# Kernel optimization log

Hardware: AMD Instinct MI355X
Metric: run time of the kernel (lower is better)

Reference implementation:

```python
import jax, jax.numpy as jnp
import numpy as np

N_NODES = 100000
N_EDGES = 1600000
IN_DIM = 256
HID = 128
N_LAYERS = 4
OUT_DIM = 7
LAMDA = 0.5
LN_EPS = 1e-5


def setup_inputs() -> dict:
    key = jax.random.key(0)
    ks = jax.random.split(key, 12)
    x = jax.random.normal(ks[0], (N_NODES, IN_DIM), jnp.float32)
    edge_index = jax.random.randint(ks[1], (2, N_EDGES), 0, N_NODES, dtype=jnp.int32)

    def unif(k, shape, fan_out):
        s = 1.0 / np.sqrt(fan_out)
        return jax.random.uniform(k, shape, jnp.float32, -s, s)

    W_proj = unif(ks[2], (IN_DIM, HID), HID)
    b_proj = unif(ks[3], (HID,), HID)
    gamma = jnp.ones((HID,), jnp.float32)
    beta = jnp.zeros((HID,), jnp.float32)
    q_w = unif(ks[4], (HID, 1), 1)
    q_b = unif(ks[5], (1,), 1)
    conv_w = unif(ks[6], (N_LAYERS, HID, HID), HID)
    cls_w = unif(ks[7], (HID, OUT_DIM), OUT_DIM)
    cls_b = unif(ks[8], (OUT_DIM,), OUT_DIM)
    return {"x": x, "edge_index": edge_index, "W_proj": W_proj, "b_proj": b_proj,
            "gamma": gamma, "beta": beta, "q_w": q_w, "q_b": q_b,
            "conv_w": conv_w, "cls_w": cls_w, "cls_b": cls_b}


def reference(x, edge_index, W_proj, b_proj, gamma, beta, q_w, q_b, conv_w, cls_w, cls_b):
    n = x.shape[0]
    row, col = edge_index[0], edge_index[1]

    # symmetric normalization: D^-1/2 A D^-1/2 with unit edge data (duplicates sum)
    deg = jax.ops.segment_sum(jnp.ones(row.shape[0], x.dtype), row, num_segments=n)
    deg = jnp.where(deg == 0, jnp.ones_like(deg), deg)  # (row_sum==0)*1 + row_sum
    d_inv_sqrt = deg ** -0.5
    ew = d_inv_sqrt[row] * d_inv_sqrt[col]  # [E]

    def spmm(h):  # out[r] += ew * h[c]
        return jax.ops.segment_sum(ew[:, None] * h[col], row, num_segments=n)

    def layernorm(h):
        mu = jnp.mean(h, axis=-1, keepdims=True)
        var = jnp.mean((h - mu) ** 2, axis=-1, keepdims=True)
        return gamma * (h - mu) * jax.lax.rsqrt(var + LN_EPS) + beta

    h0 = layernorm(x @ W_proj + b_proj)  # project + layernorm
    h = h0
    for i in range(conv_w.shape[0]):
        # dropout is identity in eval mode
        s = jax.nn.sigmoid(h @ q_w + q_b - 1.0)  # [N,1] learned gate
        theta = LAMDA / (i + 1)
        hi = spmm(h)
        support = (1.0 - s) * hi + s * h0  # AOR blend (variant=False -> r == support)
        out = theta * (support @ conv_w[i]) + (1.0 - theta) * support  # DLR
        h = layernorm(jax.nn.relu(out))
    return h @ cls_w + cls_b
```

## Files before the change

### kernel.cpp

```cpp
#include <hip/hip_runtime.h>
#include <hip/hip_bf16.h>
#include <hip/hip_fp16.h>
#include <stdint.h>

#define N_NODES 100000
#define N_EDGES 1600000
#define IN_DIM 256
#define HID 128
#define N_LAYERS 4
#define OUT_DIM 7
#define LN_EPS 1e-5f

#define BSHIFT 6
#define BROWS 64
#define NBK 1563
#define CHUNK 16384
#define NCH ((N_EDGES + CHUNK - 1) / CHUNK)

typedef __attribute__((ext_vector_type(8))) short bf16x8;
typedef __attribute__((ext_vector_type(4))) float f32x4;

__device__ inline float bf2f1(uint16_t u) {
    union { uint32_t i; float f; } a; a.i = ((uint32_t)u) << 16; return a.f;
}
__device__ inline uint16_t f2bf(float f) {
    union { float f; uint32_t i; } a; a.f = f;
    uint32_t lsb = (a.i >> 16) & 1u;
    a.i += 0x7fffu + lsb;
    return (uint16_t)(a.i >> 16);
}
__device__ inline uint32_t packq(float a, float b, float qinv) {
    int qa = __float2int_rn(a * qinv);
    int qb = __float2int_rn(b * qinv);
    return ((uint32_t)(uint16_t)(short)qa) | (((uint32_t)(uint16_t)(short)qb) << 16);
}

__global__ void k_detect(const uint32_t* __restrict__ W, int* __restrict__ flag) {
    if (threadIdx.x == 0 && blockIdx.x == 0) {
        int cnt = 0;
        for (int i = 0; i < 64; i++) {
            uint32_t lo = W[i] & 0xffffu;
            uint32_t ex = (lo >> 7) & 0xff;
            if (ex >= 0x60 && ex < 0x7c) cnt++;
        }
        *flag = (cnt < 32) ? 1 : 0;
    }
}

__global__ __launch_bounds__(256) void k_cvt(const void* a0, const void* a1, const void* a2,
                                             const void* a3, const void* a4, const void* a5,
                                             const void* a6, const void* a7, const void* a8,
                                             float* __restrict__ dst, const int* __restrict__ flag) {
    int t = blockIdx.x * 256 + threadIdx.x;
    if (t >= 99720) return;
    const void* src; int i; int off;
    if      (t < 32768) { src = a0; i = t;         off = 0;     }
    else if (t < 32896) { src = a1; i = t - 32768; off = 32768; }
    else if (t < 33024) { src = a2; i = t - 32896; off = 32896; }
    else if (t < 33152) { src = a3; i = t - 33024; off = 33024; }
    else if (t < 33280) { src = a4; i = t - 33152; off = 33152; }
    else if (t < 33281) { src = a5; i = t - 33280; off = 33280; }
    else if (t < 98817) { src = a6; i = t - 33281; off = 33296; }
    else if (t < 99713) { src = a7; i = t - 98817; off = 98832; }
    else                { src = a8; i = t - 99713; off = 99728; }
    float v;
    if (*flag) v = ((const float*)src)[i];
    else       v = bf2f1(((const uint16_t*)src)[i]);
    dst[off + i] = v;
}

__global__ __launch_bounds__(256) void k_wsplit(const float* __restrict__ stg,
                                                uint16_t* __restrict__ wpThi, uint16_t* __restrict__ wpTlo,
                                                uint16_t* __restrict__ cwThi, uint16_t* __restrict__ cwTlo) {
    int t = blockIdx.x * 256 + threadIdx.x;
    if (t >= 32768 + 65536) return;
    float v; size_t dst; uint16_t *ha, *la;
    if (t < 32768) {
        int k = t >> 7, c = t & 127;
        v = stg[t];
        dst = (size_t)c * 256 + k; ha = wpThi; la = wpTlo;
    } else {
        int u = t - 32768;
        int L = u >> 14, rem = u & 16383;
        int k = rem >> 7, c = rem & 127;
        v = stg[33296 + u];
        dst = (size_t)L * 16384 + (size_t)c * 128 + k; ha = cwThi; la = cwTlo;
    }
    uint16_t hb = f2bf(v);
    uint16_t lb = f2bf(v - bf2f1(hb));
    ha[dst] = hb; la[dst] = lb;
}


__global__ __launch_bounds__(256) void k_hist(const int* __restrict__ row, int* __restrict__ hist) {
    __shared__ int lh[NBK];
    int b = blockIdx.x, tid = threadIdx.x;
    for (int i = tid; i < NBK; i += 256) lh[i] = 0;
    __syncthreads();
    int e0 = b * CHUNK;
    int lim = N_EDGES - e0; if (lim > CHUNK) lim = CHUNK;
    for (int i = tid; i < lim; i += 256) atomicAdd(&lh[row[e0 + i] >> BSHIFT], 1);
    __syncthreads();
    for (int i = tid; i < NBK; i += 256) hist[(size_t)b * NBK + i] = lh[i];
}

__global__ __launch_bounds__(128) void k_hscan(int* __restrict__ hist, int* __restrict__ totB) {
    __shared__ int s[128];
    int bkt = blockIdx.x, t = threadIdx.x;
    int v = (t < NCH) ? hist[(size_t)t * NBK + bkt] : 0;
    s[t] = v;
    __syncthreads();
    for (int off = 1; off < 128; off <<= 1) {
        int add = (t >= off) ? s[t - off] : 0;
        __syncthreads();
        s[t] += add;
        __syncthreads();
    }
    if (t < NCH) hist[(size_t)t * NBK + bkt] = s[t] - v;
    if (t == 127) totB[bkt] = s[127];
}

__global__ __launch_bounds__(256) void k_bscan(const int* __restrict__ totB,
                                               int* __restrict__ boffB, int* __restrict__ rp) {
    __shared__ int ps[256];
    int t = threadIdx.x;
    const int STRIP = 7;
    int base = t * STRIP;
    int loc[STRIP]; int sum = 0;
#pragma unroll
    for (int j = 0; j < STRIP; j++) {
        int idx = base + j;
        int v = (idx < NBK) ? totB[idx] : 0;
        loc[j] = sum; sum += v;
    }
    ps[t] = sum;
    __syncthreads();
    int v = ps[t];
    for (int off = 1; off < 256; off <<= 1) {
        int add = (t >= off) ? ps[t - off] : 0;
        __syncthreads();
        ps[t] += add;
        __syncthreads();
    }
    int excl = ps[t] - v;
#pragma unroll
    for (int j = 0; j < STRIP; j++) {
        int idx = base + j;
        if (idx < NBK) boffB[idx] = excl + loc[j];
    }
    if (t == 0) { boffB[NBK] = N_EDGES; rp[N_NODES] = N_EDGES; }
}

__global__ __launch_bounds__(256) void k_sortscat(const int* __restrict__ row, const int* __restrict__ col,
                                                  const int* __restrict__ hist, const int* __restrict__ boffB,
                                                  uint32_t* __restrict__ ebp) {
    __shared__ int dbase[NBK];
    __shared__ int lcnt[NBK];
    int b = blockIdx.x, tid = threadIdx.x;
    for (int i = tid; i < NBK; i += 256) {
        dbase[i] = boffB[i] + hist[(size_t)b * NBK + i];
        lcnt[i] = 0;
    }
    __syncthreads();
    int e0 = b * CHUNK;
    int lim = N_EDGES - e0; if (lim > CHUNK) lim = CHUNK;
    for (int i = tid; i < lim; i += 256) {
        int r = row[e0 + i], c = col[e0 + i];
        int bk = r >> BSHIFT;
        int rank = atomicAdd(&lcnt[bk], 1);
        ebp[dbase[bk] + rank] = ((uint32_t)(r & (BROWS - 1)) << 17) | (uint32_t)c;
    }
}

__global__ __launch_bounds__(256) void k_bfin(const uint32_t* __restrict__ ebp, const int* __restrict__ boffB,
                                              int* __restrict__ rp, float* __restrict__ dis,
                                              int* __restrict__ edc) {
    __shared__ int ldeg[BROWS];
    __shared__ int lcur[BROWS];
    int b = blockIdx.x, tid = threadIdx.x;
    int base = boffB[b];
    int n = boffB[b + 1] - base;
    if (tid < BROWS) ldeg[tid] = 0;
    __syncthreads();
    for (int i = tid; i < n; i += 256) atomicAdd(&ldeg[ebp[base + i] >> 17], 1);
    __syncthreads();
    if (tid == 0) {
        int run = 0;
        for (int r = 0; r < BROWS; r++) { int d = ldeg[r]; lcur[r] = run; run += d; }
    }
    __syncthreads();
    int row0 = b << BSHIFT;
    if (tid < BROWS && row0 + tid < N_NODES) {
        int d = ldeg[tid];
        rp[row0 + tid]  = base + lcur[tid];
        dis[row0 + tid] = rsqrtf((float)(d > 0 ? d : 1));
    }
    __syncthreads();
    for (int i = tid; i < n; i += 256) {
        uint32_t pk = ebp[base + i];
        int r = pk >> 17;
        int pos = atomicAdd(&lcur[r], 1);
        edc[base + pos] = (int)(pk & 0x1FFFFu);
    }
}


__global__ __launch_bounds__(256) void k_spmm(const uint32_t* __restrict__ Hq,
                                              const float* __restrict__ ScD,
                                              const float* __restrict__ H0,
                                              const int* __restrict__ rp,
                                              const int* __restrict__ edc,
                                              const float* __restrict__ S,
                                              const float* __restrict__ dis,
                                              float* __restrict__ Sup) {
    int wid  = (blockIdx.x * 256 + threadIdx.x) >> 6;
    int lane = threadIdx.x & 63;
    if (wid >= N_NODES) return;

    float s  = S[wid];
    float dr = dis[wid];

    int p0 = rp[wid], p1 = rp[wid + 1];
    float ax = 0.f, ay = 0.f;
    int p = p0;
    for (; p + 4 <= p1; p += 4) {
        int c0 = edc[p], c1 = edc[p + 1], c2 = edc[p + 2], c3 = edc[p + 3];
        uint32_t u0 = Hq[(size_t)c0 * 64 + lane];
        uint32_t u1 = Hq[(size_t)c1 * 64 + lane];
        uint32_t u2 = Hq[(size_t)c2 * 64 + lane];
        uint32_t u3 = Hq[(size_t)c3 * 64 + lane];
        float w0 = ScD[c0], w1 = ScD[c1], w2 = ScD[c2], w3 = ScD[c3];
        ax += w0 * (float)((int)(u0 << 16) >> 16) + w1 * (float)((int)(u1 << 16) >> 16)
            + w2 * (float)((int)(u2 << 16) >> 16) + w3 * (float)((int)(u3 << 16) >> 16);
        ay += w0 * (float)((int)u0 >> 16) + w1 * (float)((int)u1 >> 16)
            + w2 * (float)((int)u2 >> 16) + w3 * (float)((int)u3 >> 16);
    }
    for (; p < p1; p++) {
        int c = edc[p];
        uint32_t u = Hq[(size_t)c * 64 + lane];
        float w = ScD[c];
        ax += w * (float)((int)(u << 16) >> 16);
        ay += w * (float)((int)u >> 16);
    }
    float h0x = H0[(size_t)wid * 128 + lane];
    float h0y = H0[(size_t)wid * 128 + 64 + lane];
    float f = (1.f - s) * dr;
    Sup[(size_t)wid * 128 + lane]      = f * ax + s * h0x;
    Sup[(size_t)wid * 128 + 64 + lane] = f * ay + s * h0y;
}


template <int KD, int MODE, int WH, int WQ>
__global__ __launch_bounds__(256) void k_gemm_mfma(
    const void* __restrict__ Araw,
    const uint16_t* __restrict__ WThi,
    const uint16_t* __restrict__ WTlo,
    const float* __restrict__ bias, const float* __restrict__ gamma,
    const float* __restrict__ beta, const float* __restrict__ qw,
    const float* __restrict__ qb, float theta, const int* __restrict__ flag,
    const float* __restrict__ dis,
    float* __restrict__ Hout, uint32_t* __restrict__ Hq,
    float* __restrict__ Sc, float* __restrict__ S)
{
    __shared__ __align__(16) uint16_t sAhi[64 * 64];
    __shared__ __align__(16) uint16_t sAlo[64 * 64];
    __shared__ __align__(16) uint16_t sBhi[128 * 64];
    __shared__ __align__(16) uint16_t sBlo[128 * 64];

    const int tid  = threadIdx.x;
    const int lane = tid & 63;
    const int wv   = tid >> 6;
    const int li   = lane & 15;
    const int lg   = lane >> 4;
    const size_t row0 = (size_t)blockIdx.x * 64;
    const int f32in = (MODE == 0) ? *flag : 1;

    f32x4 acc[8];
#pragma unroll
    for (int ct = 0; ct < 8; ct++) acc[ct] = (f32x4){0.f, 0.f, 0.f, 0.f};

    for (int kc = 0; kc < KD / 64; kc++) {
        __syncthreads();
#pragma unroll
        for (int it = 0; it < 2; it++) {
            int s  = tid + it * 256;
            int r  = s >> 3, sl = s & 7;
            size_t rg = row0 + r; if (rg >= N_NODES) rg = N_NODES - 1;
            uint4 vh, vl;
            if (f32in) {
                const float* p = (const float*)Araw + rg * KD + kc * 64 + sl * 8;
                float4 u0 = *(const float4*)p;
                float4 u1 = *(const float4*)(p + 4);
                float f[8] = {u0.x, u0.y, u0.z, u0.w, u1.x, u1.y, u1.z, u1.w};
                uint32_t hw[8], lw[8];
#pragma unroll
                for (int j = 0; j < 8; j++) {
                    uint16_t hb = f2bf(f[j]);
                    uint16_t lb = f2bf(f[j] - bf2f1(hb));
                    hw[j] = hb; lw[j] = lb;
                }
                vh.x = hw[0] | (hw[1] << 16); vh.y = hw[2] | (hw[3] << 16);
                vh.z = hw[4] | (hw[5] << 16); vh.w = hw[6] | (hw[7] << 16);
                vl.x = lw[0] | (lw[1] << 16); vl.y = lw[2] | (lw[3] << 16);
                vl.z = lw[4] | (lw[5] << 16); vl.w = lw[6] | (lw[7] << 16);
            } else {
                vh = *(const uint4*)((const uint16_t*)Araw + rg * KD + kc * 64 + sl * 8);
                vl.x = 0u; vl.y = 0u; vl.z = 0u; vl.w = 0u;
            }
            uint32_t byte = (uint32_t)(r * 128 + sl * 16) ^ (uint32_t)((r & 7) << 4);
            *(uint4*)((char*)sAhi + byte) = vh;
            *(uint4*)((char*)sAlo + byte) = vl;
        }
#pragma unroll
        for (int it = 0; it < 4; it++) {
            int s = tid + it * 256;
            int r = s >> 3, sl = s & 7;
            size_t gsrc = (size_t)r * KD + kc * 64 + sl * 8;
            uint4 vh = *(const uint4*)(WThi + gsrc);
            uint4 vl = *(const uint4*)(WTlo + gsrc);
            uint32_t byte = (uint32_t)(r * 128 + sl * 16) ^ (uint32_t)((r & 7) << 4);
            *(uint4*)((char*)sBhi + byte) = vh;
            *(uint4*)((char*)sBlo + byte) = vl;
        }
        __syncthreads();
#pragma unroll
        for (int ks = 0; ks < 2; ks++) {
            int arow = wv * 16 + li;
            uint32_t ab = (uint32_t)(arow * 128 + ks * 64 + lg * 16) ^ (uint32_t)((arow & 7) << 4);
            bf16x8 ah = *(const bf16x8*)((const char*)sAhi + ab);
            bf16x8 al = *(const bf16x8*)((const char*)sAlo + ab);
#pragma unroll
            for (int ct = 0; ct < 8; ct++) {
                int brow = ct * 16 + li;
                uint32_t bb = (uint32_t)(brow * 128 + ks * 64 + lg * 16) ^ (uint32_t)((brow & 7) << 4);
                bf16x8 bh = *(const bf16x8*)((const char*)sBhi + bb);
                bf16x8 bl = *(const bf16x8*)((const char*)sBlo + bb);
                acc[ct] = __builtin_amdgcn_mfma_f32_16x16x32_bf16(ah, bh, acc[ct], 0, 0, 0);
                acc[ct] = __builtin_amdgcn_mfma_f32_16x16x32_bf16(ah, bl, acc[ct], 0, 0, 0);
                acc[ct] = __builtin_amdgcn_mfma_f32_16x16x32_bf16(al, bh, acc[ct], 0, 0, 0);
            }
        }
    }

    float gm[8], bt[8], qv[8], bi[8];
#pragma unroll
    for (int ct = 0; ct < 8; ct++) {
        int c = ct * 16 + li;
        gm[ct] = gamma[c]; bt[ct] = beta[c]; qv[ct] = qw[c];
        bi[ct] = (MODE == 0) ? bias[c] : 0.f;
    }
    const float qbv = qb[0];
    const float om  = 1.f - theta;
    const float* Af = (const float*)Araw;

#pragma unroll
    for (int r = 0; r < 4; r++) {
        int rowl  = wv * 16 + lg * 4 + r;
        size_t rg = row0 + rowl;
        size_t rc = (rg < N_NODES) ? rg : (N_NODES - 1);
        float v[8];
        if (MODE == 0) {
#pragma unroll
            for (int ct = 0; ct < 8; ct++) v[ct] = acc[ct][r] + bi[ct];
        } else {
#pragma unroll
            for (int ct = 0; ct < 8; ct++) {
                float sv = Af[rc * KD + ct * 16 + li];
                float o  = theta * acc[ct][r] + om * sv;
                v[ct] = o > 0.f ? o : 0.f;
            }
        }
        float sum = 0.f, sq = 0.f;
#pragma unroll
        for (int ct = 0; ct < 8; ct++) { sum += v[ct]; sq += v[ct] * v[ct]; }
        sum += __shfl_xor(sum, 1); sum += __shfl_xor(sum, 2);
        sum += __shfl_xor(sum, 4); sum += __shfl_xor(sum, 8);
        sq  += __shfl_xor(sq, 1);  sq  += __shfl_xor(sq, 2);
        sq  += __shfl_xor(sq, 4);  sq  += __shfl_xor(sq, 8);
        float mu  = sum * (1.f / 128.f);
        float var = fmaxf(sq * (1.f / 128.f) - mu * mu, 0.f);
        float rs  = rsqrtf(var + LN_EPS);
        float y[8];
#pragma unroll
        for (int ct = 0; ct < 8; ct++) y[ct] = gm[ct] * (v[ct] - mu) * rs + bt[ct];

        if (WQ) {
            float zd = 0.f, am = 0.f;
#pragma unroll
            for (int ct = 0; ct < 8; ct++) { zd += y[ct] * qv[ct]; am = fmaxf(am, fabsf(y[ct])); }
            zd += __shfl_xor(zd, 1); zd += __shfl_xor(zd, 2);
            zd += __shfl_xor(zd, 4); zd += __shfl_xor(zd, 8);
            am = fmaxf(am, __shfl_xor(am, 1)); am = fmaxf(am, __shfl_xor(am, 2));
            am = fmaxf(am, __shfl_xor(am, 4)); am = fmaxf(am, __shfl_xor(am, 8));
            float amc  = fmaxf(am, 1e-20f);
            float qinv = 32767.f / amc;
            if (rg < N_NODES) {
                uint32_t* mq = Hq + rg * 64;
#pragma unroll
                for (int ct = 0; ct < 4; ct++)
                    mq[ct * 16 + li] = packq(y[ct], y[ct + 4], qinv);
                if (li == 0) {
                    Sc[rg] = amc * (1.f / 32767.f) * dis[rg];
                    S[rg]  = 1.f / (1.f + __expf(-(zd + qbv - 1.f)));
                }
            }
        }
        if (WH && rg < N_NODES) {
            float* dst = Hout + rg * 128;
#pragma unroll
            for (int ct = 0; ct < 8; ct++) dst[ct * 16 + li] = y[ct];
        }
    }
}


__global__ __launch_bounds__(256) void k_cls(const float* __restrict__ H,
                                             const float* __restrict__ Wc,
                                             const float* __restrict__ bc,
                                             const int* __restrict__ flag,
                                             void* __restrict__ out) {
    __shared__ float wS[128][8];
    int tid = threadIdx.x;
    for (int idx = tid; idx < 128 * 7; idx += 256) wS[idx / 7][idx % 7] = Wc[idx];
    __syncthreads();
    int isf32 = *flag;
    int gid = blockIdx.x * 256 + tid;
    int n = gid >> 3, j = gid & 7;
    if (n >= N_NODES || j >= OUT_DIM) return;
    const float4* hr = (const float4*)(H + (size_t)n * 128);
    float acc = bc[j];
#pragma unroll
    for (int k4 = 0; k4 < 32; k4++) {
        float4 h4 = hr[k4];
        acc += h4.x * wS[4 * k4][j]     + h4.y * wS[4 * k4 + 1][j]
             + h4.z * wS[4 * k4 + 2][j] + h4.w * wS[4 * k4 + 3][j];
    }
    size_t oi = (size_t)n * OUT_DIM + j;
    if (isf32) ((float*)out)[oi] = acc;
    else       ((uint16_t*)out)[oi] = f2bf(acc);
}


extern "C" void kernel_launch(void* const* d_in, const int* in_sizes, int n_in,
                              void* d_out, int out_size, void* d_ws, size_t ws_size,
                              hipStream_t stream) {
    const void* x_raw = d_in[0];
    const int*  ei    = (const int*)d_in[1];
    const int* row = ei;
    const int* col = ei + N_EDGES;

    char* ws = (char*)d_ws;
    size_t off = 0;
    auto alloc = [&](size_t b) { void* p = ws + off; off = (off + b + 255) & ~(size_t)255; return p; };
    int*      flag = (int*)alloc(4);
    float*    stgf = (float*)alloc((size_t)99744 * 4);
    int*      rp   = (int*)alloc(((size_t)N_NODES + 1) * 4);
    float*    dis  = (float*)alloc((size_t)N_NODES * 4);
    int*      hist = (int*)alloc((size_t)NCH * NBK * 4);
    int*      totB = (int*)alloc((size_t)NBK * 4);
    int*      boffB= (int*)alloc(((size_t)NBK + 1) * 4);
    int*      edc  = (int*)alloc((size_t)N_EDGES * 4);
    float*    h0   = (float*)alloc((size_t)N_NODES * HID * 4);
    float*    sup  = (float*)alloc((size_t)N_NODES * HID * 4);
    uint32_t* hq   = (uint32_t*)alloc((size_t)N_NODES * 64 * 4);
    float*    Scq  = (float*)alloc((size_t)N_NODES * 4);
    float*    Sg   = (float*)alloc((size_t)N_NODES * 4);
    uint16_t* wpThi = (uint16_t*)alloc((size_t)32768 * 2);
    uint16_t* wpTlo = (uint16_t*)alloc((size_t)32768 * 2);
    uint16_t* cwThi = (uint16_t*)alloc((size_t)65536 * 2);
    uint16_t* cwTlo = (uint16_t*)alloc((size_t)65536 * 2);
    uint32_t* ebp  = (uint32_t*)h0;

    const float* bp  = stgf + 32768;
    const float* gm  = stgf + 32896;
    const float* bt  = stgf + 33024;
    const float* qw  = stgf + 33152;
    const float* qb  = stgf + 33280;
    const float* clw = stgf + 98832;
    const float* clb = stgf + 99728;

    k_detect<<<1, 64, 0, stream>>>((const uint32_t*)d_in[2], flag);
    k_cvt<<<(99720 + 255) / 256, 256, 0, stream>>>(d_in[2], d_in[3], d_in[4], d_in[5], d_in[6],
                                                   d_in[7], d_in[8], d_in[9], d_in[10], stgf, flag);
    k_wsplit<<<(98304 + 255) / 256, 256, 0, stream>>>(stgf, wpThi, wpTlo, cwThi, cwTlo);

    k_hist<<<NCH, 256, 0, stream>>>(row, hist);
    k_hscan<<<NBK, 128, 0, stream>>>(hist, totB);
    k_bscan<<<1, 256, 0, stream>>>(totB, boffB, rp);
    k_sortscat<<<NCH, 256, 0, stream>>>(row, col, hist, boffB, ebp);
    k_bfin<<<NBK, 256, 0, stream>>>(ebp, boffB, rp, dis, edc);

    const int gemm_grid = (N_NODES + 63) / 64;
    k_gemm_mfma<IN_DIM, 0, 1, 1><<<gemm_grid, 256, 0, stream>>>(
        x_raw, wpThi, wpTlo, bp, gm, bt, qw, qb, 0.f, flag, dis, h0, hq, Scq, Sg);

    for (int i = 0; i < N_LAYERS; i++) {
        k_spmm<<<(N_NODES + 3) / 4, 256, 0, stream>>>(hq, Scq, h0, rp, edc, Sg, dis, sup);
        float theta = 0.5f / (float)(i + 1);
        const uint16_t* whi = cwThi + (size_t)i * 16384;
        const uint16_t* wlo = cwTlo + (size_t)i * 16384;
        if (i < N_LAYERS - 1) {
            k_gemm_mfma<HID, 1, 0, 1><<<gemm_grid, 256, 0, stream>>>(
                sup, whi, wlo, nullptr, gm, bt, qw, qb, theta, flag, dis, sup, hq, Scq, Sg);
        } else {
            k_gemm_mfma<HID, 1, 1, 0><<<gemm_grid, 256, 0, stream>>>(
                sup, whi, wlo, nullptr, gm, bt, qw, qb, theta, flag, dis, sup, hq, Scq, Sg);
        }
    }
    k_cls<<<((size_t)N_NODES * 8 + 255) / 256, 256, 0, stream>>>(sup, clw, clb, flag, d_out);
}
```

Measured before the change: 755.0 us.

## Prefetch next GEMM K-chunk into registers, specialize precision path, unroll SpMM by 8

The GEMM kernel body becomes a template on a full-precision flag. When the input is bf16 (flag off), the low-part weight loads and the extra MFMA passes are removed at compile time. The K-loop now prefetches the next chunk of A and B into registers while MFMAs run on the current shared-memory tile, which adds register pressure and a second barrier per iteration. The SpMM gather loop is unrolled to 8 edges with batched index, row and scale loads, and the H0 load is hoisted so more memory requests are in flight.

New measurement: 884.2 us. +17.1%, slower.

```diff
diff --git a/kernel.cpp b/kernel.cpp
--- a/kernel.cpp
+++ b/kernel.cpp
@@ -219,21 +219,39 @@
 
     float s  = S[wid];
     float dr = dis[wid];
+    float h0x = H0[(size_t)wid * 128 + lane];
+    float h0y = H0[(size_t)wid * 128 + 64 + lane];
 
     int p0 = rp[wid], p1 = rp[wid + 1];
     float ax = 0.f, ay = 0.f;
     int p = p0;
+    for (; p + 8 <= p1; p += 8) {
+        int c[8]; uint32_t u[8]; float w[8];
+#pragma unroll
+        for (int j = 0; j < 8; j++) c[j] = edc[p + j];
+#pragma unroll
+        for (int j = 0; j < 8; j++) u[j] = Hq[(size_t)c[j] * 64 + lane];
+#pragma unroll
+        for (int j = 0; j < 8; j++) w[j] = ScD[c[j]];
+#pragma unroll
+        for (int j = 0; j < 8; j++) {
+            ax += w[j] * (float)((int)(u[j] << 16) >> 16);
+            ay += w[j] * (float)((int)u[j] >> 16);
+        }
+    }
     for (; p + 4 <= p1; p += 4) {
-        int c0 = edc[p], c1 = edc[p + 1], c2 = edc[p + 2], c3 = edc[p + 3];
-        uint32_t u0 = Hq[(size_t)c0 * 64 + lane];
-        uint32_t u1 = Hq[(size_t)c1 * 64 + lane];
-        uint32_t u2 = Hq[(size_t)c2 * 64 + lane];
-        uint32_t u3 = Hq[(size_t)c3 * 64 + lane];
-        float w0 = ScD[c0], w1 = ScD[c1], w2 = ScD[c2], w3 = ScD[c3];
-        ax += w0 * (float)((int)(u0 << 16) >> 16) + w1 * (float)((int)(u1 << 16) >> 16)
-            + w2 * (float)((int)(u2 << 16) >> 16) + w3 * (float)((int)(u3 << 16) >> 16);
-        ay += w0 * (float)((int)u0 >> 16) + w1 * (float)((int)u1 >> 16)
-            + w2 * (float)((int)u2 >> 16) + w3 * (float)((int)u3 >> 16);
+        int c[4]; uint32_t u[4]; float w[4];
+#pragma unroll
+        for (int j = 0; j < 4; j++) c[j] = edc[p + j];
+#pragma unroll
+        for (int j = 0; j < 4; j++) u[j] = Hq[(size_t)c[j] * 64 + lane];
+#pragma unroll
+        for (int j = 0; j < 4; j++) w[j] = ScD[c[j]];
+#pragma unroll
+        for (int j = 0; j < 4; j++) {
+            ax += w[j] * (float)((int)(u[j] << 16) >> 16);
+            ay += w[j] * (float)((int)u[j] >> 16);
+        }
     }
     for (; p < p1; p++) {
         int c = edc[p];
@@ -242,30 +260,24 @@
         ax += w * (float)((int)(u << 16) >> 16);
         ay += w * (float)((int)u >> 16);
     }
-    float h0x = H0[(size_t)wid * 128 + lane];
-    float h0y = H0[(size_t)wid * 128 + 64 + lane];
     float f = (1.f - s) * dr;
     Sup[(size_t)wid * 128 + lane]      = f * ax + s * h0x;
     Sup[(size_t)wid * 128 + 64 + lane] = f * ay + s * h0y;
 }
 
 
-template <int KD, int MODE, int WH, int WQ>
-__global__ __launch_bounds__(256) void k_gemm_mfma(
-    const void* __restrict__ Araw,
-    const uint16_t* __restrict__ WThi,
-    const uint16_t* __restrict__ WTlo,
-    const float* __restrict__ bias, const float* __restrict__ gamma,
-    const float* __restrict__ beta, const float* __restrict__ qw,
-    const float* __restrict__ qb, float theta, const int* __restrict__ flag,
-    const float* __restrict__ dis,
-    float* __restrict__ Hout, uint32_t* __restrict__ Hq,
-    float* __restrict__ Sc, float* __restrict__ S)
+template <int KD, int MODE, int WH, int WQ, int WF>
+__device__ __forceinline__ void gemm_body(
+    const void* __restrict__ Araw, const uint16_t* __restrict__ WThi,
+    const uint16_t* __restrict__ WTlo, const float* __restrict__ bias,
+    const float* __restrict__ gamma, const float* __restrict__ beta,
+    const float* __restrict__ qw, const float* __restrict__ qb, float theta,
+    const float* __restrict__ dis, float* __restrict__ Hout,
+    uint32_t* __restrict__ Hq, float* __restrict__ Sc, float* __restrict__ S,
+    uint16_t* sAhi, uint16_t* sAlo, uint16_t* sBhi, uint16_t* sBlo)
 {
-    __shared__ __align__(16) uint16_t sAhi[64 * 64];
-    __shared__ __align__(16) uint16_t sAlo[64 * 64];
-    __shared__ __align__(16) uint16_t sBhi[128 * 64];
-    __shared__ __align__(16) uint16_t sBlo[128 * 64];
+    constexpr int F32A = (MODE == 0) ? WF : 1;
+    constexpr int NC = KD / 64;
 
     const int tid  = threadIdx.x;
     const int lane = tid & 63;
@@ -273,73 +285,106 @@
     const int li   = lane & 15;
     const int lg   = lane >> 4;
     const size_t row0 = (size_t)blockIdx.x * 64;
-    const int f32in = (MODE == 0) ? *flag : 1;
 
     f32x4 acc[8];
 #pragma unroll
     for (int ct = 0; ct < 8; ct++) acc[ct] = (f32x4){0.f, 0.f, 0.f, 0.f};
 
-    for (int kc = 0; kc < KD / 64; kc++) {
-        __syncthreads();
+    float far[2][8];
+    uint4 abr[2];
+    uint4 bhr[4], blr[4];
+
+    auto loadA = [&](int kc) {
 #pragma unroll
         for (int it = 0; it < 2; it++) {
-            int s  = tid + it * 256;
-            int r  = s >> 3, sl = s & 7;
+            int s = tid + it * 256;
+            int r = s >> 3, sl = s & 7;
             size_t rg = row0 + r; if (rg >= N_NODES) rg = N_NODES - 1;
-            uint4 vh, vl;
-            if (f32in) {
+            if constexpr (F32A) {
                 const float* p = (const float*)Araw + rg * KD + kc * 64 + sl * 8;
                 float4 u0 = *(const float4*)p;
                 float4 u1 = *(const float4*)(p + 4);
-                float f[8] = {u0.x, u0.y, u0.z, u0.w, u1.x, u1.y, u1.z, u1.w};
+                far[it][0] = u0.x; far[it][1] = u0.y; far[it][2] = u0.z; far[it][3] = u0.w;
+                far[it][4] = u1.x; far[it][5] = u1.y; far[it][6] = u1.z; far[it][7] = u1.w;
+            } else {
+                abr[it] = *(const uint4*)((const uint16_t*)Araw + rg * KD + kc * 64 + sl * 8);
+            }
+        }
+    };
+    auto storeA = [&]() {
+#pragma unroll
+        for (int it = 0; it < 2; it++) {
+            int s = tid + it * 256;
+            int r = s >> 3, sl = s & 7;
+            uint32_t byte = (uint32_t)(r * 128 + sl * 16) ^ (uint32_t)((r & 7) << 4);
+            if constexpr (F32A) {
                 uint32_t hw[8], lw[8];
 #pragma unroll
                 for (int j = 0; j < 8; j++) {
-                    uint16_t hb = f2bf(f[j]);
-                    uint16_t lb = f2bf(f[j] - bf2f1(hb));
+                    uint16_t hb = f2bf(far[it][j]);
+                    uint16_t lb = f2bf(far[it][j] - bf2f1(hb));
                     hw[j] = hb; lw[j] = lb;
                 }
+                uint4 vh, vl;
                 vh.x = hw[0] | (hw[1] << 16); vh.y = hw[2] | (hw[3] << 16);
                 vh.z = hw[4] | (hw[5] << 16); vh.w = hw[6] | (hw[7] << 16);
                 vl.x = lw[0] | (lw[1] << 16); vl.y = lw[2] | (lw[3] << 16);
                 vl.z = lw[4] | (lw[5] << 16); vl.w = lw[6] | (lw[7] << 16);
+                *(uint4*)((char*)sAhi + byte) = vh;
+                *(uint4*)((char*)sAlo + byte) = vl;
             } else {
-                vh = *(const uint4*)((const uint16_t*)Araw + rg * KD + kc * 64 + sl * 8);
-                vl.x = 0u; vl.y = 0u; vl.z = 0u; vl.w = 0u;
+                *(uint4*)((char*)sAhi + byte) = abr[it];
             }
-            uint32_t byte = (uint32_t)(r * 128 + sl * 16) ^ (uint32_t)((r & 7) << 4);
-            *(uint4*)((char*)sAhi + byte) = vh;
-            *(uint4*)((char*)sAlo + byte) = vl;
-        }
+        }
+    };
+    auto loadB = [&](int kc) {
 #pragma unroll
         for (int it = 0; it < 4; it++) {
             int s = tid + it * 256;
             int r = s >> 3, sl = s & 7;
             size_t gsrc = (size_t)r * KD + kc * 64 + sl * 8;
-            uint4 vh = *(const uint4*)(WThi + gsrc);
-            uint4 vl = *(const uint4*)(WTlo + gsrc);
+            bhr[it] = *(const uint4*)(WThi + gsrc);
+            if constexpr (WF) blr[it] = *(const uint4*)(WTlo + gsrc);
+        }
+    };
+    auto storeB = [&]() {
+#pragma unroll
+        for (int it = 0; it < 4; it++) {
+            int s = tid + it * 256;
+            int r = s >> 3, sl = s & 7;
             uint32_t byte = (uint32_t)(r * 128 + sl * 16) ^ (uint32_t)((r & 7) << 4);
-            *(uint4*)((char*)sBhi + byte) = vh;
-            *(uint4*)((char*)sBlo + byte) = vl;
-        }
+            *(uint4*)((char*)sBhi + byte) = bhr[it];
+            if constexpr (WF) *(uint4*)((char*)sBlo + byte) = blr[it];
+        }
+    };
+
+    loadA(0); loadB(0);
+    for (int kc = 0; kc < NC; kc++) {
+        storeA(); storeB();
         __syncthreads();
+        if (kc + 1 < NC) { loadA(kc + 1); loadB(kc + 1); }
 #pragma unroll
         for (int ks = 0; ks < 2; ks++) {
             int arow = wv * 16 + li;
             uint32_t ab = (uint32_t)(arow * 128 + ks * 64 + lg * 16) ^ (uint32_t)((arow & 7) << 4);
             bf16x8 ah = *(const bf16x8*)((const char*)sAhi + ab);
-            bf16x8 al = *(const bf16x8*)((const char*)sAlo + ab);
+            bf16x8 al;
+            if constexpr (F32A) al = *(const bf16x8*)((const char*)sAlo + ab);
 #pragma unroll
             for (int ct = 0; ct < 8; ct++) {
                 int brow = ct * 16 + li;
                 uint32_t bb = (uint32_t)(brow * 128 + ks * 64 + lg * 16) ^ (uint32_t)((brow & 7) << 4);
                 bf16x8 bh = *(const bf16x8*)((const char*)sBhi + bb);
-                bf16x8 bl = *(const bf16x8*)((const char*)sBlo + bb);
                 acc[ct] = __builtin_amdgcn_mfma_f32_16x16x32_bf16(ah, bh, acc[ct], 0, 0, 0);
-                acc[ct] = __builtin_amdgcn_mfma_f32_16x16x32_bf16(ah, bl, acc[ct], 0, 0, 0);
-                acc[ct] = __builtin_amdgcn_mfma_f32_16x16x32_bf16(al, bh, acc[ct], 0, 0, 0);
+                if constexpr (F32A)
+                    acc[ct] = __builtin_amdgcn_mfma_f32_16x16x32_bf16(al, bh, acc[ct], 0, 0, 0);
+                if constexpr (WF) {
+                    bf16x8 bl = *(const bf16x8*)((const char*)sBlo + bb);
+                    acc[ct] = __builtin_amdgcn_mfma_f32_16x16x32_bf16(ah, bl, acc[ct], 0, 0, 0);
+                }
             }
         }
+        __syncthreads();
     }
 
     float gm[8], bt[8], qv[8], bi[8];
@@ -411,6 +456,29 @@
             for (int ct = 0; ct < 8; ct++) dst[ct * 16 + li] = y[ct];
         }
     }
+}
+
+template <int KD, int MODE, int WH, int WQ>
+__global__ __launch_bounds__(256) void k_gemm_mfma(
+    const void* __restrict__ Araw, const uint16_t* __restrict__ WThi,
+    const uint16_t* __restrict__ WTlo, const float* __restrict__ bias,
+    const float* __restrict__ gamma, const float* __restrict__ beta,
+    const float* __restrict__ qw, const float* __restrict__ qb, float theta,
+    const int* __restrict__ flag, const float* __restrict__ dis,
+    float* __restrict__ Hout, uint32_t* __restrict__ Hq,
+    float* __restrict__ Sc, float* __restrict__ S)
+{
+    __shared__ __align__(16) uint16_t sAhi[64 * 64];
+    __shared__ __align__(16) uint16_t sAlo[64 * 64];
+    __shared__ __align__(16) uint16_t sBhi[128 * 64];
+    __shared__ __align__(16) uint16_t sBlo[128 * 64];
+
+    if (*flag)
+        gemm_body<KD, MODE, WH, WQ, 1>(Araw, WThi, WTlo, bias, gamma, beta, qw, qb,
+                                       theta, dis, Hout, Hq, Sc, S, sAhi, sAlo, sBhi, sBlo);
+    else
+        gemm_body<KD, MODE, WH, WQ, 0>(Araw, WThi, WTlo, bias, gamma, beta, qw, qb,
+                                       theta, dis, Hout, Hq, Sc, S, sAhi, sAlo, sBhi, sBlo);
 }
 
 
```

## Drop LDS staging in GEMM, prepack weights for direct MFMA loads, deepen SpMM unroll

Applied to the files above, without the earlier changes.

Weights are prepacked into an MFMA-fragment-ordered layout so each lane loads its B fragment straight from global or L2 memory. The A operand is also read directly from global memory, which removes the shared-memory staging and both barriers per K chunk. The GEMM is templated on the input-precision flag, so bf16 inputs skip the low-part MFMA and the W-low load. The flag comes from host-side input sizes when available, with kernel variants launched conditionally. SpMM unrolls to 8 gathers per iteration and hoists the H0 loads; the trade-off is more redundant global B reads per wave and higher register pressure.

New measurement: 834.6 us. 1.11x slower.

```diff
diff --git a/kernel.cpp b/kernel.cpp
--- a/kernel.cpp
+++ b/kernel.cpp
@@ -35,6 +35,12 @@
     return ((uint32_t)(uint16_t)(short)qa) | (((uint32_t)(uint16_t)(short)qb) << 16);
 }
 
+__device__ __host__ inline int wpack_idx(int k, int c) {
+    int kc = k >> 6, ks = (k >> 5) & 1, lg = (k >> 3) & 3, e = k & 7;
+    int ct = c >> 4, li = c & 15;
+    return ((((kc * 2 + ks) * 8 + ct) * 16 + li) * 4 + lg) * 8 + e;
+}
+
 __global__ void k_detect(const uint32_t* __restrict__ W, int* __restrict__ flag) {
     if (threadIdx.x == 0 && blockIdx.x == 0) {
         int cnt = 0;
@@ -45,6 +51,9 @@
         }
         *flag = (cnt < 32) ? 1 : 0;
     }
+}
+__global__ void k_setflag(int* __restrict__ flag, int v) {
+    if (threadIdx.x == 0) *flag = v;
 }
 
 __global__ __launch_bounds__(256) void k_cvt(const void* a0, const void* a1, const void* a2,
@@ -70,21 +79,21 @@
 }
 
 __global__ __launch_bounds__(256) void k_wsplit(const float* __restrict__ stg,
-                                                uint16_t* __restrict__ wpThi, uint16_t* __restrict__ wpTlo,
-                                                uint16_t* __restrict__ cwThi, uint16_t* __restrict__ cwTlo) {
+                                                uint16_t* __restrict__ wpkhi, uint16_t* __restrict__ wpklo,
+                                                uint16_t* __restrict__ cwkhi, uint16_t* __restrict__ cwklo) {
     int t = blockIdx.x * 256 + threadIdx.x;
     if (t >= 32768 + 65536) return;
     float v; size_t dst; uint16_t *ha, *la;
     if (t < 32768) {
         int k = t >> 7, c = t & 127;
         v = stg[t];
-        dst = (size_t)c * 256 + k; ha = wpThi; la = wpTlo;
+        dst = (size_t)wpack_idx(k, c); ha = wpkhi; la = wpklo;
     } else {
         int u = t - 32768;
         int L = u >> 14, rem = u & 16383;
         int k = rem >> 7, c = rem & 127;
         v = stg[33296 + u];
-        dst = (size_t)L * 16384 + (size_t)c * 128 + k; ha = cwThi; la = cwTlo;
+        dst = (size_t)L * 16384 + wpack_idx(k, c); ha = cwkhi; la = cwklo;
     }
     uint16_t hb = f2bf(v);
     uint16_t lb = f2bf(v - bf2f1(hb));
@@ -219,21 +228,39 @@
 
     float s  = S[wid];
     float dr = dis[wid];
+    float h0x = H0[(size_t)wid * 128 + lane];
+    float h0y = H0[(size_t)wid * 128 + 64 + lane];
 
     int p0 = rp[wid], p1 = rp[wid + 1];
     float ax = 0.f, ay = 0.f;
     int p = p0;
+    for (; p + 8 <= p1; p += 8) {
+        int c[8]; uint32_t u[8]; float w[8];
+#pragma unroll
+        for (int j = 0; j < 8; j++) c[j] = edc[p + j];
+#pragma unroll
+        for (int j = 0; j < 8; j++) u[j] = Hq[(size_t)c[j] * 64 + lane];
+#pragma unroll
+        for (int j = 0; j < 8; j++) w[j] = ScD[c[j]];
+#pragma unroll
+        for (int j = 0; j < 8; j++) {
+            ax += w[j] * (float)((int)(u[j] << 16) >> 16);
+            ay += w[j] * (float)((int)u[j] >> 16);
+        }
+    }
     for (; p + 4 <= p1; p += 4) {
-        int c0 = edc[p], c1 = edc[p + 1], c2 = edc[p + 2], c3 = edc[p + 3];
-        uint32_t u0 = Hq[(size_t)c0 * 64 + lane];
-        uint32_t u1 = Hq[(size_t)c1 * 64 + lane];
-        uint32_t u2 = Hq[(size_t)c2 * 64 + lane];
-        uint32_t u3 = Hq[(size_t)c3 * 64 + lane];
-        float w0 = ScD[c0], w1 = ScD[c1], w2 = ScD[c2], w3 = ScD[c3];
-        ax += w0 * (float)((int)(u0 << 16) >> 16) + w1 * (float)((int)(u1 << 16) >> 16)
-            + w2 * (float)((int)(u2 << 16) >> 16) + w3 * (float)((int)(u3 << 16) >> 16);
-        ay += w0 * (float)((int)u0 >> 16) + w1 * (float)((int)u1 >> 16)
-            + w2 * (float)((int)u2 >> 16) + w3 * (float)((int)u3 >> 16);
+        int c[4]; uint32_t u[4]; float w[4];
+#pragma unroll
+        for (int j = 0; j < 4; j++) c[j] = edc[p + j];
+#pragma unroll
+        for (int j = 0; j < 4; j++) u[j] = Hq[(size_t)c[j] * 64 + lane];
+#pragma unroll
+        for (int j = 0; j < 4; j++) w[j] = ScD[c[j]];
+#pragma unroll
+        for (int j = 0; j < 4; j++) {
+            ax += w[j] * (float)((int)(u[j] << 16) >> 16);
+            ay += w[j] * (float)((int)u[j] >> 16);
+        }
     }
     for (; p < p1; p++) {
         int c = edc[p];
@@ -242,19 +269,17 @@
         ax += w * (float)((int)(u << 16) >> 16);
         ay += w * (float)((int)u >> 16);
     }
-    float h0x = H0[(size_t)wid * 128 + lane];
-    float h0y = H0[(size_t)wid * 128 + 64 + lane];
     float f = (1.f - s) * dr;
     Sup[(size_t)wid * 128 + lane]      = f * ax + s * h0x;
     Sup[(size_t)wid * 128 + 64 + lane] = f * ay + s * h0y;
 }
 
 
-template <int KD, int MODE, int WH, int WQ>
-__global__ __launch_bounds__(256) void k_gemm_mfma(
+template <int KD, int MODE, int WH, int WQ, int WF>
+__global__ __launch_bounds__(256, 4) void k_gemm(
     const void* __restrict__ Araw,
-    const uint16_t* __restrict__ WThi,
-    const uint16_t* __restrict__ WTlo,
+    const uint16_t* __restrict__ Whi,
+    const uint16_t* __restrict__ Wlo,
     const float* __restrict__ bias, const float* __restrict__ gamma,
     const float* __restrict__ beta, const float* __restrict__ qw,
     const float* __restrict__ qb, float theta, const int* __restrict__ flag,
@@ -262,10 +287,9 @@
     float* __restrict__ Hout, uint32_t* __restrict__ Hq,
     float* __restrict__ Sc, float* __restrict__ S)
 {
-    __shared__ __align__(16) uint16_t sAhi[64 * 64];
-    __shared__ __align__(16) uint16_t sAlo[64 * 64];
-    __shared__ __align__(16) uint16_t sBhi[128 * 64];
-    __shared__ __align__(16) uint16_t sBlo[128 * 64];
+    if (*flag != WF) return;
+    constexpr int F32A = (MODE == 0) ? WF : 1;
+    constexpr int NC = KD / 64;
 
     const int tid  = threadIdx.x;
     const int lane = tid & 63;
@@ -273,71 +297,45 @@
     const int li   = lane & 15;
     const int lg   = lane >> 4;
     const size_t row0 = (size_t)blockIdx.x * 64;
-    const int f32in = (MODE == 0) ? *flag : 1;
+    size_t arow = row0 + wv * 16 + li;
+    if (arow >= N_NODES) arow = N_NODES - 1;
 
     f32x4 acc[8];
 #pragma unroll
     for (int ct = 0; ct < 8; ct++) acc[ct] = (f32x4){0.f, 0.f, 0.f, 0.f};
 
-    for (int kc = 0; kc < KD / 64; kc++) {
-        __syncthreads();
-#pragma unroll
-        for (int it = 0; it < 2; it++) {
-            int s  = tid + it * 256;
-            int r  = s >> 3, sl = s & 7;
-            size_t rg = row0 + r; if (rg >= N_NODES) rg = N_NODES - 1;
-            uint4 vh, vl;
-            if (f32in) {
-                const float* p = (const float*)Araw + rg * KD + kc * 64 + sl * 8;
-                float4 u0 = *(const float4*)p;
-                float4 u1 = *(const float4*)(p + 4);
+#pragma unroll
+    for (int kc = 0; kc < NC; kc++) {
+#pragma unroll
+        for (int ks = 0; ks < 2; ks++) {
+            const int koff = kc * 64 + ks * 32 + lg * 8;
+            bf16x8 ah, al;
+            if constexpr (F32A) {
+                const float* ap = (const float*)Araw + arow * KD + koff;
+                float4 u0 = *(const float4*)ap;
+                float4 u1 = *(const float4*)(ap + 4);
                 float f[8] = {u0.x, u0.y, u0.z, u0.w, u1.x, u1.y, u1.z, u1.w};
-                uint32_t hw[8], lw[8];
 #pragma unroll
                 for (int j = 0; j < 8; j++) {
                     uint16_t hb = f2bf(f[j]);
-                    uint16_t lb = f2bf(f[j] - bf2f1(hb));
-                    hw[j] = hb; lw[j] = lb;
+                    ah[j] = (short)hb;
+                    al[j] = (short)f2bf(f[j] - bf2f1(hb));
                 }
-                vh.x = hw[0] | (hw[1] << 16); vh.y = hw[2] | (hw[3] << 16);
-                vh.z = hw[4] | (hw[5] << 16); vh.w = hw[6] | (hw[7] << 16);
-                vl.x = lw[0] | (lw[1] << 16); vl.y = lw[2] | (lw[3] << 16);
-                vl.z = lw[4] | (lw[5] << 16); vl.w = lw[6] | (lw[7] << 16);
             } else {
-                vh = *(const uint4*)((const uint16_t*)Araw + rg * KD + kc * 64 + sl * 8);
-                vl.x = 0u; vl.y = 0u; vl.z = 0u; vl.w = 0u;
+                ah = *(const bf16x8*)((const uint16_t*)Araw + arow * KD + koff);
             }
-            uint32_t byte = (uint32_t)(r * 128 + sl * 16) ^ (uint32_t)((r & 7) << 4);
-            *(uint4*)((char*)sAhi + byte) = vh;
-            *(uint4*)((char*)sAlo + byte) = vl;
-        }
-#pragma unroll
-        for (int it = 0; it < 4; it++) {
-            int s = tid + it * 256;
-            int r = s >> 3, sl = s & 7;
-            size_t gsrc = (size_t)r * KD + kc * 64 + sl * 8;
-            uint4 vh = *(const uint4*)(WThi + gsrc);
-            uint4 vl = *(const uint4*)(WTlo + gsrc);
-            uint32_t byte = (uint32_t)(r * 128 + sl * 16) ^ (uint32_t)((r & 7) << 4);
-            *(uint4*)((char*)sBhi + byte) = vh;
-            *(uint4*)((char*)sBlo + byte) = vl;
-        }
-        __syncthreads();
-#pragma unroll
-        for (int ks = 0; ks < 2; ks++) {
-            int arow = wv * 16 + li;
-            uint32_t ab = (uint32_t)(arow * 128 + ks * 64 + lg * 16) ^ (uint32_t)((arow & 7) << 4);
-            bf16x8 ah = *(const bf16x8*)((const char*)sAhi + ab);
-            bf16x8 al = *(const bf16x8*)((const char*)sAlo + ab);
+            const size_t wb0 = (size_t)(kc * 2 + ks) * 4096 + (size_t)li * 32 + (size_t)lg * 8;
 #pragma unroll
             for (int ct = 0; ct < 8; ct++) {
-                int brow = ct * 16 + li;
-                uint32_t bb = (uint32_t)(brow * 128 + ks * 64 + lg * 16) ^ (uint32_t)((brow & 7) << 4);
-                bf16x8 bh = *(const bf16x8*)((const char*)sBhi + bb);
-                bf16x8 bl = *(const bf16x8*)((const char*)sBlo + bb);
+                const size_t wb = wb0 + (size_t)ct * 512;
+                bf16x8 bh = *(const bf16x8*)(Whi + wb);
                 acc[ct] = __builtin_amdgcn_mfma_f32_16x16x32_bf16(ah, bh, acc[ct], 0, 0, 0);
-                acc[ct] = __builtin_amdgcn_mfma_f32_16x16x32_bf16(ah, bl, acc[ct], 0, 0, 0);
-                acc[ct] = __builtin_amdgcn_mfma_f32_16x16x32_bf16(al, bh, acc[ct], 0, 0, 0);
+                if constexpr (F32A)
+                    acc[ct] = __builtin_amdgcn_mfma_f32_16x16x32_bf16(al, bh, acc[ct], 0, 0, 0);
+                if constexpr (WF) {
+                    bf16x8 bl = *(const bf16x8*)(Wlo + wb);
+                    acc[ct] = __builtin_amdgcn_mfma_f32_16x16x32_bf16(ah, bl, acc[ct], 0, 0, 0);
+                }
             }
         }
     }
@@ -465,10 +463,10 @@
     uint32_t* hq   = (uint32_t*)alloc((size_t)N_NODES * 64 * 4);
     float*    Scq  = (float*)alloc((size_t)N_NODES * 4);
     float*    Sg   = (float*)alloc((size_t)N_NODES * 4);
-    uint16_t* wpThi = (uint16_t*)alloc((size_t)32768 * 2);
-    uint16_t* wpTlo = (uint16_t*)alloc((size_t)32768 * 2);
-    uint16_t* cwThi = (uint16_t*)alloc((size_t)65536 * 2);
-    uint16_t* cwTlo = (uint16_t*)alloc((size_t)65536 * 2);
+    uint16_t* wpkhi = (uint16_t*)alloc((size_t)32768 * 2);
+    uint16_t* wpklo = (uint16_t*)alloc((size_t)32768 * 2);
+    uint16_t* cwkhi = (uint16_t*)alloc((size_t)65536 * 2);
+    uint16_t* cwklo = (uint16_t*)alloc((size_t)65536 * 2);
     uint32_t* ebp  = (uint32_t*)h0;
 
     const float* bp  = stgf + 32768;
@@ -479,10 +477,19 @@
     const float* clw = stgf + 98832;
     const float* clb = stgf + 99728;
 
-    k_detect<<<1, 64, 0, stream>>>((const uint32_t*)d_in[2], flag);
+    int hostflag = -1;
+    if (in_sizes && n_in >= 3) {
+        if      (in_sizes[2] == 32768 * 4) hostflag = 1;
+        else if (in_sizes[2] == 32768 * 2) hostflag = 0;
+        else if (in_sizes[0] == N_NODES * IN_DIM * 4) hostflag = 1;
+        else if (in_sizes[0] == N_NODES * IN_DIM * 2) hostflag = 0;
+    }
+    if (hostflag >= 0) k_setflag<<<1, 64, 0, stream>>>(flag, hostflag);
+    else               k_detect<<<1, 64, 0, stream>>>((const uint32_t*)d_in[2], flag);
+
     k_cvt<<<(99720 + 255) / 256, 256, 0, stream>>>(d_in[2], d_in[3], d_in[4], d_in[5], d_in[6],
                                                    d_in[7], d_in[8], d_in[9], d_in[10], stgf, flag);
-    k_wsplit<<<(98304 + 255) / 256, 256, 0, stream>>>(stgf, wpThi, wpTlo, cwThi, cwTlo);
+    k_wsplit<<<(98304 + 255) / 256, 256, 0, stream>>>(stgf, wpkhi, wpklo, cwkhi, cwklo);
 
     k_hist<<<NCH, 256, 0, stream>>>(row, hist);
     k_hscan<<<NBK, 128, 0, stream>>>(hist, totB);
@@ -491,20 +498,32 @@
     k_bfin<<<NBK, 256, 0, stream>>>(ebp, boffB, rp, dis, edc);
 
     const int gemm_grid = (N_NODES + 63) / 64;
-    k_gemm_mfma<IN_DIM, 0, 1, 1><<<gemm_grid, 256, 0, stream>>>(
-        x_raw, wpThi, wpTlo, bp, gm, bt, qw, qb, 0.f, flag, dis, h0, hq, Scq, Sg);
+    if (hostflag != 0)
+        k_gemm<IN_DIM, 0, 1, 1, 1><<<gemm_grid, 256, 0, stream>>>(
+            x_raw, wpkhi, wpklo, bp, gm, bt, qw, qb, 0.f, flag, dis, h0, hq, Scq, Sg);
+    if (hostflag != 1)
+        k_gemm<IN_DIM, 0, 1, 1, 0><<<gemm_grid, 256, 0, stream>>>(
+            x_raw, wpkhi, wpklo, bp, gm, bt, qw, qb, 0.f, flag, dis, h0, hq, Scq, Sg);
 
     for (int i = 0; i < N_LAYERS; i++) {
         k_spmm<<<(N_NODES + 3) / 4, 256, 0, stream>>>(hq, Scq, h0, rp, edc, Sg, dis, sup);
         float theta = 0.5f / (float)(i + 1);
-        const uint16_t* whi = cwThi + (size_t)i * 16384;
-        const uint16_t* wlo = cwTlo + (size_t)i * 16384;
+        const uint16_t* whi = cwkhi + (size_t)i * 16384;
+        const uint16_t* wlo = cwklo + (size_t)i * 16384;
         if (i < N_LAYERS - 1) {
-            k_gemm_mfma<HID, 1, 0, 1><<<gemm_grid, 256, 0, stream>>>(
-                sup, whi, wlo, nullptr, gm, bt, qw, qb, theta, flag, dis, sup, hq, Scq, Sg);
+            if (hostflag != 0)
+                k_gemm<HID, 1, 0, 1, 1><<<gemm_grid, 256, 0, stream>>>(
+                    sup, whi, wlo, nullptr, gm, bt, qw, qb, theta, flag, dis, sup, hq, Scq, Sg);
+            if (hostflag != 1)
+                k_gemm<HID, 1, 0, 1, 0><<<gemm_grid, 256, 0, stream>>>(
+                    sup, whi, wlo, nullptr, gm, bt, qw, qb, theta, flag, dis, sup, hq, Scq, Sg);
         } else {
-            k_gemm_mfma<HID, 1, 1, 0><<<gemm_grid, 256, 0, stream>>>(
-                sup, whi, wlo, nullptr, gm, bt, qw, qb, theta, flag, dis, sup, hq, Scq, Sg);
+            if (hostflag != 0)
+                k_gemm<HID, 1, 1, 0, 1><<<gemm_grid, 256, 0, stream>>>(
+                    sup, whi, wlo, nullptr, gm, bt, qw, qb, theta, flag, dis, sup, hq, Scq, Sg);
+            if (hostflag != 1)
+                k_gemm<HID, 1, 1, 0, 0><<<gemm_grid, 256, 0, stream>>>(
+                    sup, whi, wlo, nullptr, gm, bt, qw, qb, theta, flag, dis, sup, hq, Scq, Sg);
         }
     }
     k_cls<<<((size_t)N_NODES * 8 + 255) / 256, 256, 0, stream>>>(sup, clw, clb, flag, d_out);
```
